# Kernel optimization log

Measured on AMD Instinct MI355X. Metric: run time of the kernel, lower is better.

Reference implementation:

```python
import jax, jax.numpy as jnp
import numpy as np

B, T, D = 32, 1024, 384
T_OUT = 4096  # static padded output length (= target_len for every batch element)


def setup_inputs() -> dict:
    key = jax.random.key(0)
    k1, k2 = jax.random.split(key)
    x = jax.random.normal(k1, (B, T, D), dtype=jnp.float32)
    durations = jax.random.randint(k2, (B, T), 0, 8, dtype=jnp.int32)
    # constant target length -> torch pads/truncates every row to T_OUT,
    # and max over batch is T_OUT, so output is [B, T_OUT, D].
    target_len = jnp.full((B,), T_OUT, dtype=jnp.int32)
    return {"x": x, "durations": durations, "target_len": target_len}


def reference(x, durations, target_len):
    # x: [B, T, D]; durations: [B, T] int; target_len: [B] int.
    # Ragged repeat-expansion expressed as cumulative-duration searchsorted + gather.
    Bx, Tx, Dx = x.shape
    dur = jnp.maximum(durations, 0)
    ends = jnp.cumsum(dur, axis=1)              # [B, T] exclusive-end frame index per token
    total = ends[:, -1]                          # [B] total expanded length per batch row
    pos = jnp.arange(T_OUT, dtype=ends.dtype)    # [T_OUT] output frame positions
    # token index owning each output frame: number of ends <= pos
    idx = jax.vmap(lambda e: jnp.searchsorted(e, pos, side="right"))(ends)  # [B, T_OUT]
    idx = jnp.clip(idx, 0, Tx - 1)
    out = jnp.take_along_axis(x, idx[..., None], axis=1)  # [B, T_OUT, D]
    # frames past min(total_expansion, target_len) are zero padding (truncate + pad semantics)
    limit = jnp.minimum(total, target_len.astype(total.dtype))  # [B]
    valid = pos[None, :] < limit[:, None]                        # [B, T_OUT]
    return jnp.where(valid[..., None], out, jnp.zeros((), x.dtype))
```

## Files before the change

### kernel.cpp

```cpp
#include <hip/hip_runtime.h>


#define BB 32
#define TT 1024
#define DD 384
#define TOUT 4096
#define D4 (DD / 4)

__global__ __launch_bounds__(1024) void lr_scan_scatter(
    const int* __restrict__ dur,
    const int* __restrict__ target_len,
    int* __restrict__ idx,
    int* __restrict__ limit)
{
    __shared__ int s[TT];
    const int b = blockIdx.x;
    const int t = threadIdx.x;

    int d = dur[b * TT + t];
    d = d > 0 ? d : 0;
    s[t] = d;
    __syncthreads();

    #pragma unroll
    for (int off = 1; off < TT; off <<= 1) {
        int v = (t >= off) ? s[t - off] : 0;
        __syncthreads();
        s[t] += v;
        __syncthreads();
    }

    const int e  = s[t];
    const int st = (t == 0) ? 0 : s[t - 1];

    if (t == TT - 1) {
        const int tot = e;
        const int tl  = target_len[b];
        limit[b] = tot < tl ? tot : tl;
    }

    const int e2 = e < TOUT ? e : TOUT;
    const int s2 = st < TOUT ? st : TOUT;
    for (int p = s2; p < e2; ++p) {
        idx[b * TOUT + p] = t;
    }
}

__global__ __launch_bounds__(256) void lr_gather(
    const float4* __restrict__ x,
    const int* __restrict__ idx,
    const int* __restrict__ limit,
    float4* __restrict__ out)
{
    const int b = blockIdx.y;
    const int r = blockIdx.x * 256 + threadIdx.x;
    const int p = r / D4;
    const int c = r - p * D4;

    const int lim = limit[b];
    float4 v = make_float4(0.f, 0.f, 0.f, 0.f);
    if (p < lim) {
        int t = idx[b * TOUT + p];
        t = t < 0 ? 0 : (t > TT - 1 ? TT - 1 : t);
        v = x[(b * TT + t) * D4 + c];
    }
    out[(b * TOUT + p) * D4 + c] = v;
}

extern "C" void kernel_launch(void* const* d_in, const int* in_sizes, int n_in,
                              void* d_out, int out_size, void* d_ws, size_t ws_size,
                              hipStream_t stream) {
    const float* x        = (const float*)d_in[0];
    const int* durations  = (const int*)d_in[1];
    const int* target_len = (const int*)d_in[2];
    float* out            = (float*)d_out;

    int* limit = (int*)d_ws;
    int* idx   = (int*)d_ws + 64;

    lr_scan_scatter<<<BB, TT, 0, stream>>>(durations, target_len, idx, limit);

    dim3 grid((TOUT * D4) / 256, BB);
    lr_gather<<<grid, 256, 0, stream>>>((const float4*)x, idx, limit, (float4*)out);
}
```

Baseline: 249.8 us.

## Build idx via binary search with sentinel; widen gather to 64B per thread

The index kernel now does a 4-wide per-thread scan over 256 threads. Each output position is then resolved by a shared-memory binary search instead of a per-token scatter loop, and past-limit positions are encoded as -1, which removes the separate limit buffer. The gather kernel has each thread copy four float4 vectors (64 bytes) with nontemporal stores, giving fewer threads and fewer index loads. The aim is to cut the serial imbalance in the scatter and raise store efficiency on the bandwidth-bound gather, at the cost of fewer resident threads in flight.

```diff
diff --git a/kernel.cpp b/kernel.cpp
--- a/kernel.cpp
+++ b/kernel.cpp
@@ -7,64 +7,90 @@
 #define TOUT 4096
 #define D4 (DD / 4)
 
-__global__ __launch_bounds__(1024) void lr_scan_scatter(
-    const int* __restrict__ dur,
+typedef float v4f __attribute__((ext_vector_type(4)));
+
+__global__ __launch_bounds__(256) void lr_build_idx(
+    const int4* __restrict__ dur4,
     const int* __restrict__ target_len,
-    int* __restrict__ idx,
-    int* __restrict__ limit)
+    int* __restrict__ idx)
 {
-    __shared__ int s[TT];
+    __shared__ int ends[TT];
+    __shared__ int sums[256];
+    __shared__ int s_limit;
     const int b = blockIdx.x;
-    const int t = threadIdx.x;
+    const int q = threadIdx.x;
 
-    int d = dur[b * TT + t];
-    d = d > 0 ? d : 0;
-    s[t] = d;
+    int4 d = dur4[b * 256 + q];
+    const int d0 = d.x > 0 ? d.x : 0;
+    const int d1 = d.y > 0 ? d.y : 0;
+    const int d2 = d.z > 0 ? d.z : 0;
+    const int d3 = d.w > 0 ? d.w : 0;
+    const int e0 = d0, e1 = e0 + d1, e2 = e1 + d2, e3 = e2 + d3;
+    sums[q] = e3;
     __syncthreads();
 
     #pragma unroll
-    for (int off = 1; off < TT; off <<= 1) {
-        int v = (t >= off) ? s[t - off] : 0;
+    for (int off = 1; off < 256; off <<= 1) {
+        int u = (q >= off) ? sums[q - off] : 0;
         __syncthreads();
-        s[t] += v;
+        sums[q] += u;
         __syncthreads();
     }
+    const int base = sums[q] - e3;
+    ((int4*)ends)[q] = make_int4(base + e0, base + e1, base + e2, base + e3);
 
-    const int e  = s[t];
-    const int st = (t == 0) ? 0 : s[t - 1];
+    if (q == 255) {
+        const int total = base + e3;
+        const int tl = target_len[b];
+        s_limit = total < tl ? total : tl;
+    }
+    __syncthreads();
 
-    if (t == TT - 1) {
-        const int tot = e;
-        const int tl  = target_len[b];
-        limit[b] = tot < tl ? tot : tl;
+    const int lim = s_limit;
+    int lo[16];
+    #pragma unroll
+    for (int k = 0; k < 16; ++k) lo[k] = 0;
+    #pragma unroll
+    for (int s = 512; s > 0; s >>= 1) {
+        #pragma unroll
+        for (int k = 0; k < 16; ++k) {
+            const int p = q + 256 * k;
+            lo[k] += (ends[lo[k] + s - 1] <= p) ? s : 0;
+        }
     }
-
-    const int e2 = e < TOUT ? e : TOUT;
-    const int s2 = st < TOUT ? st : TOUT;
-    for (int p = s2; p < e2; ++p) {
-        idx[b * TOUT + p] = t;
+    #pragma unroll
+    for (int k = 0; k < 16; ++k) {
+        const int p = q + 256 * k;
+        int t = lo[k] > TT - 1 ? TT - 1 : lo[k];
+        idx[b * TOUT + p] = (p < lim) ? t : -1;
     }
 }
 
 __global__ __launch_bounds__(256) void lr_gather(
-    const float4* __restrict__ x,
+    const v4f* __restrict__ x,
     const int* __restrict__ idx,
-    const int* __restrict__ limit,
-    float4* __restrict__ out)
+    v4f* __restrict__ out)
 {
     const int b = blockIdx.y;
     const int r = blockIdx.x * 256 + threadIdx.x;
-    const int p = r / D4;
-    const int c = r - p * D4;
+    const int p = r / 24;
+    const int c4 = (r - p * 24) << 2;
 
-    const int lim = limit[b];
-    float4 v = make_float4(0.f, 0.f, 0.f, 0.f);
-    if (p < lim) {
-        int t = idx[b * TOUT + p];
-        t = t < 0 ? 0 : (t > TT - 1 ? TT - 1 : t);
-        v = x[(b * TT + t) * D4 + c];
+    const int t = idx[b * TOUT + p];
+    v4f v0 = (v4f)(0.f);
+    v4f v1 = v0, v2 = v0, v3 = v0;
+    if (t >= 0) {
+        const v4f* __restrict__ row = x + (b * TT + t) * D4 + c4;
+        v0 = row[0];
+        v1 = row[1];
+        v2 = row[2];
+        v3 = row[3];
     }
-    out[(b * TOUT + p) * D4 + c] = v;
+    v4f* o = out + (b * TOUT + p) * D4 + c4;
+    __builtin_nontemporal_store(v0, o + 0);
+    __builtin_nontemporal_store(v1, o + 1);
+    __builtin_nontemporal_store(v2, o + 2);
+    __builtin_nontemporal_store(v3, o + 3);
 }
 
 extern "C" void kernel_launch(void* const* d_in, const int* in_sizes, int n_in,
@@ -75,11 +101,10 @@
     const int* target_len = (const int*)d_in[2];
     float* out            = (float*)d_out;
 
-    int* limit = (int*)d_ws;
-    int* idx   = (int*)d_ws + 64;
+    int* idx = (int*)d_ws;
 
-    lr_scan_scatter<<<BB, TT, 0, stream>>>(durations, target_len, idx, limit);
+    lr_build_idx<<<BB, 256, 0, stream>>>((const int4*)durations, target_len, idx);
 
-    dim3 grid((TOUT * D4) / 256, BB);
-    lr_gather<<<grid, 256, 0, stream>>>((const float4*)x, idx, limit, (float4*)out);
+    dim3 grid((TOUT * 24) / 256, BB);
+    lr_gather<<<grid, 256, 0, stream>>>((const v4f*)x, idx, (v4f*)out);
 }
```

Result: slower. 341.8 us (+36.8%).
